# Performance work log

Hardware: AMD Instinct MI355X
Metric: run time of the kernel (lower is better)

Reference implementation:

```python
import jax, jax.numpy as jnp
import numpy as np


def setup_inputs() -> dict:
    key = jax.random.key(0)
    B, L, D, N = 2, 2048, 1024, 16
    ks = jax.random.split(key, 8)
    s = 1.0 / np.sqrt(D)
    # S4D-real init for A_log, matching the module
    A_log = jnp.log(jnp.broadcast_to(jnp.arange(1, N + 1, dtype=jnp.float32), (D, N)))
    return {
        "x": jax.random.normal(ks[0], (B, L, D), jnp.float32),
        "Wz": jax.random.normal(ks[1], (D, D), jnp.float32) * s,
        "bz": jnp.zeros((D,), jnp.float32),
        "Wx": jax.random.normal(ks[2], (D, D), jnp.float32) * s,
        "bx": jnp.zeros((D,), jnp.float32),
        "WB": jax.random.normal(ks[3], (D, N), jnp.float32) * s,
        "bB": jnp.zeros((N,), jnp.float32),
        "WC": jax.random.normal(ks[4], (D, N), jnp.float32) * s,
        "bC": jnp.zeros((N,), jnp.float32),
        "Wdt": jax.random.normal(ks[5], (D, D), jnp.float32) * s,
        "bdt": jnp.zeros((D,), jnp.float32),
        "A_log": A_log,
        "Wout": jax.random.normal(ks[6], (D, D), jnp.float32) * s,
        "bout": jnp.zeros((D,), jnp.float32),
    }


def reference(x, Wz, bz, Wx, bx, WB, bB, WC, bC, Wdt, bdt, A_log, Wout, bout):
    B, L, D = x.shape
    N = A_log.shape[1]

    # input-dependent projections
    z = jax.nn.sigmoid(x @ Wz + bz)            # (B,L,D) gate
    x_ssm = x @ Wx + bx                        # (B,L,D)
    Bm = x @ WB + bB                           # (B,L,N)
    C = x @ WC + bC                            # (B,L,N)
    dt = jax.nn.softplus(x @ Wdt + bdt)        # (B,L,D)

    A = -jnp.exp(A_log)                        # (D,N)
    A_bar = jnp.exp(dt[..., None] * A)         # (B,L,D,N) discretized state matrix
    # x_db = x_ssm * (dt * B)  -> (B,L,D,N)
    x_db = x_ssm[..., None] * (dt[..., None] * Bm[..., None, :])

    # scan over time: move L to leading axis
    a_scan = jnp.transpose(A_bar, (1, 0, 2, 3))   # (L,B,D,N)
    x_scan = jnp.transpose(x_db, (1, 0, 2, 3))    # (L,B,D,N)
    c_scan = jnp.transpose(C, (1, 0, 2))          # (L,B,N)

    def ssm_step(h, inp):
        a_t, x_t, c_t = inp                       # (B,D,N),(B,D,N),(B,N)
        h_new = a_t * h + x_t
        y_t = jnp.einsum('bdn,bn->bd', h_new, c_t)
        return h_new, y_t

    h0 = jnp.zeros((B, D, N), x.dtype)
    _, y_ssm = jax.lax.scan(ssm_step, h0, (a_scan, x_scan, c_scan))
    y_ssm = jnp.transpose(y_ssm, (1, 0, 2))       # (B,L,D)

    y = y_ssm * z
    return y @ Wout + bout
```

## Files before the change

kernel.cpp:

```cpp
#include <hip/hip_runtime.h>
#include <math.h>

#define CHUNKS 64
#define LCH    32

#define GBM 128
#define GBN 128
#define GBK 32
#define ATILE (GBM * GBK)
#define BTILE (GBN * GBK)

typedef __attribute__((ext_vector_type(8))) short bf16x8;
typedef __attribute__((ext_vector_type(4))) float f32x4;
typedef __attribute__((ext_vector_type(8))) unsigned short us8;
typedef __attribute__((ext_vector_type(4))) unsigned short us4;

typedef __attribute__((address_space(1))) const unsigned int gu32;
typedef __attribute__((address_space(3))) unsigned int lu32;

__device__ __forceinline__ void gload16(const unsigned short* g, unsigned short* l) {
    __builtin_amdgcn_global_load_lds((gu32*)g, (lu32*)l, 16, 0, 0);
}

__device__ __forceinline__ unsigned short f2bf(float f) {
    unsigned int u = __float_as_uint(f);
    unsigned int r = (u + 0x7FFFu + ((u >> 16) & 1u)) >> 16;
    return (unsigned short)r;
}

__global__ __launch_bounds__(256) void convert_bf16(
    const float* __restrict__ in, unsigned short* __restrict__ out, int n4)
{
    int i = blockIdx.x * 256 + threadIdx.x;
    if (i < n4) {
        float4 v = ((const float4*)in)[i];
        us4 u;
        u[0] = f2bf(v.x); u[1] = f2bf(v.y); u[2] = f2bf(v.z); u[3] = f2bf(v.w);
        ((us4*)out)[i] = u;
    }
}

__global__ __launch_bounds__(256) void transpose4_bf16(
    const float* __restrict__ W0, const float* __restrict__ W1,
    const float* __restrict__ W2, const float* __restrict__ W3,
    unsigned short* __restrict__ T0, unsigned short* __restrict__ T1,
    unsigned short* __restrict__ T2, unsigned short* __restrict__ T3, int D)
{
    const float* W = (blockIdx.z == 0) ? W0 : (blockIdx.z == 1) ? W1
                   : (blockIdx.z == 2) ? W2 : W3;
    unsigned short* Wt = (blockIdx.z == 0) ? T0 : (blockIdx.z == 1) ? T1
                       : (blockIdx.z == 2) ? T2 : T3;

    __shared__ float Ls[64][65];
    const int n0 = blockIdx.x * 64;
    const int k0 = blockIdx.y * 64;
    const int tx = threadIdx.x;

#pragma unroll
    for (int i = 0; i < 4; i++) {
        int idx = tx + i * 256;
        int kr = idx >> 4;
        int ng = idx & 15;
        float4 v = *(const float4*)&W[(size_t)(k0 + kr) * D + n0 + ng * 4];
        Ls[kr][ng * 4 + 0] = v.x;
        Ls[kr][ng * 4 + 1] = v.y;
        Ls[kr][ng * 4 + 2] = v.z;
        Ls[kr][ng * 4 + 3] = v.w;
    }
    __syncthreads();
#pragma unroll
    for (int i = 0; i < 4; i++) {
        int idx = tx + i * 256;
        int nr = idx >> 4;
        int kg = idx & 15;
        us4 u;
#pragma unroll
        for (int j = 0; j < 4; j++) u[j] = f2bf(Ls[kg * 4 + j][nr]);
        *(us4*)&Wt[(size_t)(n0 + nr) * D + k0 + kg * 4] = u;
    }
}

__device__ __forceinline__ void stage_tile(
    const unsigned short* __restrict__ A, const unsigned short* __restrict__ B,
    unsigned short* As, unsigned short* Bs,
    int brow, int bcol, int K, int k0, int wave, int srow, int sq)
{
    gload16(&A[(size_t)(brow + wave * 32      + srow) * K + k0 + sq],
            &As[(wave * 32) * GBK]);
    gload16(&A[(size_t)(brow + wave * 32 + 16 + srow) * K + k0 + sq],
            &As[(wave * 32 + 16) * GBK]);
    gload16(&B[(size_t)(bcol + wave * 32      + srow) * K + k0 + sq],
            &Bs[(wave * 32) * GBK]);
    gload16(&B[(size_t)(bcol + wave * 32 + 16 + srow) * K + k0 + sq],
            &Bs[(wave * 32 + 16) * GBK]);
}

__device__ __forceinline__ void gemm_core(
    const unsigned short* __restrict__ A, const unsigned short* __restrict__ B,
    unsigned short* As, unsigned short* Bs,
    int brow, int bcol, int K, f32x4 acc[4][4],
    int wave, int lane, int wr, int wc, int lrow, int lk)
{
    const int srow = lane >> 2;
    const int sq   = ((lane & 3) ^ ((lane >> 3) & 3)) * 8;

#pragma unroll
    for (int m = 0; m < 4; m++)
#pragma unroll
        for (int n = 0; n < 4; n++) acc[m][n] = (f32x4)(0.f);

    const int nk = K / GBK;
    stage_tile(A, B, As,         Bs,         brow, bcol, K, 0,   wave, srow, sq);
    stage_tile(A, B, As + ATILE, Bs + BTILE, brow, bcol, K, GBK, wave, srow, sq);

    int cur = 0;
    int nxt = 2;
    for (int kt = 0; kt < nk; ++kt) {
        if (kt + 2 < nk) {
            stage_tile(A, B, As + nxt * ATILE, Bs + nxt * BTILE,
                       brow, bcol, K, (kt + 2) * GBK, wave, srow, sq);
            asm volatile("s_waitcnt vmcnt(8)" ::: "memory");
        } else if (kt + 1 < nk) {
            asm volatile("s_waitcnt vmcnt(4)" ::: "memory");
        } else {
            asm volatile("s_waitcnt vmcnt(0)" ::: "memory");
        }
        __builtin_amdgcn_s_barrier();

        const unsigned short* as = As + cur * ATILE;
        const unsigned short* bs = Bs + cur * BTILE;

        bf16x8 av[4], bv[4];
#pragma unroll
        for (int m = 0; m < 4; m++) {
            int row = wr * 64 + m * 16 + lrow;
            av[m] = *(const bf16x8*)&as[row * GBK + ((lk ^ ((row >> 1) & 3)) * 8)];
        }
#pragma unroll
        for (int n = 0; n < 4; n++) {
            int row = wc * 64 + n * 16 + lrow;
            bv[n] = *(const bf16x8*)&bs[row * GBK + ((lk ^ ((row >> 1) & 3)) * 8)];
        }
#pragma unroll
        for (int m = 0; m < 4; m++)
#pragma unroll
            for (int n = 0; n < 4; n++)
                acc[m][n] = __builtin_amdgcn_mfma_f32_16x16x32_bf16(
                    av[m], bv[n], acc[m][n], 0, 0, 0);

        asm volatile("s_waitcnt lgkmcnt(0)" ::: "memory");
        __builtin_amdgcn_s_barrier();
        cur = (cur == 2) ? 0 : cur + 1;
        nxt = (nxt == 2) ? 0 : nxt + 1;
    }
}

__global__ __launch_bounds__(256) void proj3_gemm(
    const unsigned short* __restrict__ A,
    const unsigned short* __restrict__ W0, const unsigned short* __restrict__ W1,
    const unsigned short* __restrict__ W2,
    const float* __restrict__ b0, const float* __restrict__ b1,
    const float* __restrict__ b2,
    float* __restrict__ o0, float* __restrict__ o1, float* __restrict__ o2,
    int K, int Nc)
{
    __shared__ unsigned short As[3 * ATILE];
    __shared__ unsigned short Bs[3 * BTILE];

    const int bid = blockIdx.x;
    const int idx = bid >> 3;
    const int by  = (bid & 7) * 4 + idx / 24;
    const int bx  = idx % 24;

    const int widx = bx >> 3;
    const unsigned short* B = (widx == 0) ? W0 : (widx == 1) ? W1 : W2;
    const float* bias = (widx == 0) ? b0 : (widx == 1) ? b1 : b2;
    float* out = (widx == 0) ? o0 : (widx == 1) ? o1 : o2;

    const int tx = threadIdx.x;
    const int wave = tx >> 6;
    const int lane = tx & 63;
    const int wr = wave >> 1, wc = wave & 1;
    const int lrow = lane & 15, lk = lane >> 4;
    const int brow = by * GBM;
    const int bcol = (bx & 7) * GBN;

    f32x4 acc[4][4];
    gemm_core(A, B, As, Bs, brow, bcol, K, acc, wave, lane, wr, wc, lrow, lk);

#pragma unroll
    for (int n = 0; n < 4; n++) {
        int col = bcol + wc * 64 + n * 16 + lrow;
        float bval = bias[col];
#pragma unroll
        for (int m = 0; m < 4; m++) {
#pragma unroll
            for (int r = 0; r < 4; r++) {
                int row = brow + wr * 64 + m * 16 + lk * 4 + r;
                float v = acc[m][n][r] + bval;
                if (widx == 0) v = 1.f / (1.f + __expf(-v));
                else if (widx == 2) v = (v > 20.f) ? v : log1pf(__expf(v));
                out[(size_t)row * Nc + col] = v;
            }
        }
    }
}

__global__ __launch_bounds__(256) void gemm_bt(
    const unsigned short* __restrict__ A, const unsigned short* __restrict__ B,
    const float* __restrict__ bias, float* __restrict__ out, int K, int ldo)
{
    __shared__ unsigned short As[3 * ATILE];
    __shared__ unsigned short Bs[3 * BTILE];

    const int bid = blockIdx.x;
    const int idx = bid >> 3;
    const int by  = (bid & 7) * 4 + idx / 8;
    const int bx  = idx % 8;

    const int tx = threadIdx.x;
    const int wave = tx >> 6;
    const int lane = tx & 63;
    const int wr = wave >> 1, wc = wave & 1;
    const int lrow = lane & 15, lk = lane >> 4;
    const int brow = by * GBM;
    const int bcol = bx * GBN;

    f32x4 acc[4][4];
    gemm_core(A, B, As, Bs, brow, bcol, K, acc, wave, lane, wr, wc, lrow, lk);

#pragma unroll
    for (int n = 0; n < 4; n++) {
        int col = bcol + wc * 64 + n * 16 + lrow;
        float bval = bias[col];
#pragma unroll
        for (int m = 0; m < 4; m++) {
#pragma unroll
            for (int r = 0; r < 4; r++) {
                int row = brow + wr * 64 + m * 16 + lk * 4 + r;
                out[(size_t)row * ldo + col] = acc[m][n][r] + bval;
            }
        }
    }
}

__global__ __launch_bounds__(256) void bc_proj(
    const float* __restrict__ x,
    const float* __restrict__ WB, const float* __restrict__ bB,
    const float* __restrict__ WC, const float* __restrict__ bC,
    float* __restrict__ BC, int K, int M)
{
    __shared__ unsigned short Wl[32 * 1024];

    const int tx = threadIdx.x;

#pragma unroll
    for (int i = 0; i < 16; i++) {
        int e = tx + i * 256;
        int k = e >> 2;
        int n0 = (e & 3) * 4;
        float4 v = ((const float4*)WB)[e];
        float vv[4] = {v.x, v.y, v.z, v.w};
#pragma unroll
        for (int j = 0; j < 4; j++) {
            int n = n0 + j;
            Wl[n * 1024 + (((k & ~7) ^ ((n & 15) << 3)) | (k & 7))] = f2bf(vv[j]);
        }
    }
#pragma unroll
    for (int i = 0; i < 16; i++) {
        int e = tx + i * 256;
        int k = e >> 2;
        int n0 = (e & 3) * 4;
        float4 v = ((const float4*)WC)[e];
        float vv[4] = {v.x, v.y, v.z, v.w};
#pragma unroll
        for (int j = 0; j < 4; j++) {
            int n = 16 + n0 + j;
            Wl[n * 1024 + (((k & ~7) ^ ((n & 15) << 3)) | (k & 7))] = f2bf(vv[j]);
        }
    }
    __syncthreads();

    const int n = tx & 31;
    const int r = tx >> 5;
    const int row = blockIdx.x * 8 + r;

    const unsigned short* wrow = &Wl[n * 1024];
    const int sw = (n & 15) << 3;
    const float* xrow = &x[(size_t)row * K];

    float acc = 0.f;
    for (int kb = 0; kb < K; kb += 8) {
        us8 w8 = *(const us8*)&wrow[kb ^ sw];
        float4 xa = *(const float4*)&xrow[kb];
        float4 xb = *(const float4*)&xrow[kb + 4];
        float xv[8] = {xa.x, xa.y, xa.z, xa.w, xb.x, xb.y, xb.z, xb.w};
#pragma unroll
        for (int j = 0; j < 8; j++) {
            acc = fmaf(xv[j], __uint_as_float((unsigned)(unsigned short)w8[j] << 16), acc);
        }
    }

    float bias = (n < 16) ? bB[n] : bC[n - 16];
    BC[(size_t)row * 32 + n] = acc + bias;
}

__global__ __launch_bounds__(256) void scan_phase1(
    const float* __restrict__ xs, const float* __restrict__ dt,
    const float* __restrict__ BC, const float* __restrict__ A_log,
    float* __restrict__ P, float* __restrict__ Hl, int L, int D, int M)
{
    const int tx = threadIdx.x;
    const int d  = blockIdx.x * 256 + tx;
    const int c  = blockIdx.y;
    const int b  = blockIdx.z;
    const int m0 = b * L + c * LCH;

    __shared__ float bcs[LCH][32];
    {
        int row = tx >> 3, col = (tx & 7) * 4;
        *(f32x4*)&bcs[row][col] = *(const f32x4*)&BC[(size_t)(m0 + row) * 32 + col];
    }
    __syncthreads();

    float Av[16];
#pragma unroll
    for (int i = 0; i < 4; i++) {
        f32x4 a4 = *(const f32x4*)&A_log[d * 16 + i * 4];
#pragma unroll
        for (int j = 0; j < 4; j++) Av[i * 4 + j] = -__expf(a4[j]);
    }

    float h[16];
#pragma unroll
    for (int n = 0; n < 16; n++) h[n] = 0.f;
    float dts = 0.f;

    const size_t base = (size_t)m0 * D + d;
    float dtv = dt[base], xv = xs[base];
    for (int t = 0; t < LCH; t++) {
        float dtn = 0.f, xvn = 0.f;
        if (t + 1 < LCH) {
            dtn = dt[base + (size_t)(t + 1) * D];
            xvn = xs[base + (size_t)(t + 1) * D];
        }
        float xdt = xv * dtv;
        dts += dtv;
        f32x4 bm[4];
#pragma unroll
        for (int i = 0; i < 4; i++) bm[i] = *(const f32x4*)&bcs[t][i * 4];
#pragma unroll
        for (int n = 0; n < 16; n++) {
            float a = __expf(dtv * Av[n]);
            h[n] = fmaf(a, h[n], xdt * bm[n >> 2][n & 3]);
        }
        dtv = dtn; xv = xvn;
    }

    size_t idx = (((size_t)b * D + d) * CHUNKS + c) * 16;
#pragma unroll
    for (int i = 0; i < 4; i++) {
        f32x4 p4, h4;
#pragma unroll
        for (int j = 0; j < 4; j++) {
            p4[j] = __expf(Av[i * 4 + j] * dts);
            h4[j] = h[i * 4 + j];
        }
        *(f32x4*)&P[idx + i * 4]  = p4;
        *(f32x4*)&Hl[idx + i * 4] = h4;
    }
}

__global__ __launch_bounds__(256) void scan_phase2(
    const float* __restrict__ P, float* __restrict__ Hl, int D, int N)
{
    const int tid = blockIdx.x * 256 + threadIdx.x;
    const int n = tid & 15;
    const int dd = (tid >> 4) & 1023;
    const int b = tid >> 14;

    size_t base = (((size_t)b * D + dd) * CHUNKS) * 16 + n;
    float run = 0.f;
#pragma unroll 4
    for (int c = 0; c < CHUNKS; c++) {
        float p   = P[base + (size_t)c * 16];
        float tmp = Hl[base + (size_t)c * 16];
        Hl[base + (size_t)c * 16] = run;
        run = fmaf(p, run, tmp);
    }
}

__global__ __launch_bounds__(256) void scan_phase3(
    const float* __restrict__ xs, const float* __restrict__ dt,
    const float* __restrict__ BC, const float* __restrict__ z,
    const float* __restrict__ A_log, const float* __restrict__ Hin,
    unsigned short* __restrict__ ybf, int L, int D, int M)
{
    const int tx = threadIdx.x;
    const int d  = blockIdx.x * 256 + tx;
    const int c  = blockIdx.y;
    const int b  = blockIdx.z;
    const int m0 = b * L + c * LCH;

    __shared__ float bcs[LCH][32];
    {
        int row = tx >> 3, col = (tx & 7) * 4;
        *(f32x4*)&bcs[row][col] = *(const f32x4*)&BC[(size_t)(m0 + row) * 32 + col];
    }
    __syncthreads();

    float Av[16];
#pragma unroll
    for (int i = 0; i < 4; i++) {
        f32x4 a4 = *(const f32x4*)&A_log[d * 16 + i * 4];
#pragma unroll
        for (int j = 0; j < 4; j++) Av[i * 4 + j] = -__expf(a4[j]);
    }

    float h[16];
    {
        size_t hidx = (((size_t)b * D + d) * CHUNKS + c) * 16;
#pragma unroll
        for (int i = 0; i < 4; i++) {
            f32x4 h4 = *(const f32x4*)&Hin[hidx + i * 4];
#pragma unroll
            for (int j = 0; j < 4; j++) h[i * 4 + j] = h4[j];
        }
    }

    const size_t base = (size_t)m0 * D + d;
    float dtv = dt[base], xv = xs[base], zv = z[base];
    for (int t = 0; t < LCH; t++) {
        float dtn = 0.f, xvn = 0.f, zvn = 0.f;
        if (t + 1 < LCH) {
            dtn = dt[base + (size_t)(t + 1) * D];
            xvn = xs[base + (size_t)(t + 1) * D];
            zvn = z[base + (size_t)(t + 1) * D];
        }
        float xdt = xv * dtv;
        f32x4 bm[4], cm[4];
#pragma unroll
        for (int i = 0; i < 4; i++) {
            bm[i] = *(const f32x4*)&bcs[t][i * 4];
            cm[i] = *(const f32x4*)&bcs[t][16 + i * 4];
        }
        float y = 0.f;
#pragma unroll
        for (int n = 0; n < 16; n++) {
            float a = __expf(dtv * Av[n]);
            h[n] = fmaf(a, h[n], xdt * bm[n >> 2][n & 3]);
            y = fmaf(h[n], cm[n >> 2][n & 3], y);
        }
        ybf[base + (size_t)t * D] = f2bf(y * zv);
        dtv = dtn; xv = xvn; zv = zvn;
    }
}

extern "C" void kernel_launch(void* const* d_in, const int* in_sizes, int n_in,
                              void* d_out, int out_size, void* d_ws, size_t ws_size,
                              hipStream_t stream) {
    const float* x     = (const float*)d_in[0];
    const float* Wz    = (const float*)d_in[1];
    const float* bz    = (const float*)d_in[2];
    const float* Wx    = (const float*)d_in[3];
    const float* bx    = (const float*)d_in[4];
    const float* WB    = (const float*)d_in[5];
    const float* bB    = (const float*)d_in[6];
    const float* WC    = (const float*)d_in[7];
    const float* bC    = (const float*)d_in[8];
    const float* Wdt   = (const float*)d_in[9];
    const float* bdt   = (const float*)d_in[10];
    const float* A_log = (const float*)d_in[11];
    const float* Wout  = (const float*)d_in[12];
    const float* bout  = (const float*)d_in[13];
    float* out = (float*)d_out;

    const int Bb = 2, L = 2048, D = 1024, N = 16;
    const int M = Bb * L;
    const size_t MD = (size_t)M * D;

    float* ws   = (float*)d_ws;
    float* xsb  = ws;
    float* dtb  = xsb + MD;
    float* BCb  = dtb + MD;
    float* Pb   = BCb + (size_t)M * 32;
    float* Hlb  = Pb  + (size_t)Bb * D * CHUNKS * 16;
    unsigned short* xbf   = (unsigned short*)(Hlb + (size_t)Bb * D * CHUNKS * 16);
    unsigned short* Wzt   = xbf + MD;
    unsigned short* Wxt   = Wzt + (size_t)D * D;
    unsigned short* Wdtt  = Wxt + (size_t)D * D;
    unsigned short* Woutt = Wdtt + (size_t)D * D;
    float* zb = out;

    dim3 blk(256);
    dim3 gridT(D / 64, D / 64, 4);

    convert_bf16<<<dim3((unsigned)(MD / 4 / 256)), blk, 0, stream>>>(x, xbf, (int)(MD / 4));
    transpose4_bf16<<<gridT, blk, 0, stream>>>(Wz, Wx, Wdt, Wout,
                                               Wzt, Wxt, Wdtt, Woutt, D);

    proj3_gemm<<<dim3(3 * (D / GBN) * (M / GBM)), blk, 0, stream>>>(
        xbf, Wzt, Wxt, Wdtt, bz, bx, bdt, zb, xsb, dtb, D, D);
    bc_proj<<<dim3(M / 8), blk, 0, stream>>>(x, WB, bB, WC, bC, BCb, D, M);

    dim3 gridScan(D / 256, CHUNKS, Bb);
    scan_phase1<<<gridScan, blk, 0, stream>>>(xsb, dtb, BCb, A_log, Pb, Hlb, L, D, M);
    scan_phase2<<<dim3(Bb * D * N / 256), blk, 0, stream>>>(Pb, Hlb, D, N);
    scan_phase3<<<gridScan, blk, 0, stream>>>(xsb, dtb, BCb, zb, A_log, Hlb,
                                              xbf , L, D, M);

    gemm_bt<<<dim3((D / GBN) * (M / GBM)), blk, 0, stream>>>(xbf, Woutt, bout, out, D, D);
}
```

Measured before the change: 166.6 us.

## Store projection intermediates as bf16 and fuse x conversion into bc_proj

The z, x_ssm and dt intermediates written by the projection GEMM are now stored as bf16 instead of fp32, which halves the bytes written there and read back by the scan phases. The separate fp32-to-bf16 conversion kernel for x is removed, and bc_proj now does that conversion while it already reads x, so it must launch before the projection GEMM. This saves one launch and one pass over x, at the cost of lower precision on dt and x_ssm feeding the recurrence, which could push error closer to tolerance.

```diff
diff --git a/kernel.cpp b/kernel.cpp
--- a/kernel.cpp
+++ b/kernel.cpp
@@ -27,17 +27,8 @@
     unsigned int r = (u + 0x7FFFu + ((u >> 16) & 1u)) >> 16;
     return (unsigned short)r;
 }
-
-__global__ __launch_bounds__(256) void convert_bf16(
-    const float* __restrict__ in, unsigned short* __restrict__ out, int n4)
-{
-    int i = blockIdx.x * 256 + threadIdx.x;
-    if (i < n4) {
-        float4 v = ((const float4*)in)[i];
-        us4 u;
-        u[0] = f2bf(v.x); u[1] = f2bf(v.y); u[2] = f2bf(v.z); u[3] = f2bf(v.w);
-        ((us4*)out)[i] = u;
-    }
+__device__ __forceinline__ float bf2f(unsigned short u) {
+    return __uint_as_float((unsigned)u << 16);
 }
 
 __global__ __launch_bounds__(256) void transpose4_bf16(
@@ -161,7 +152,8 @@
     const unsigned short* __restrict__ W2,
     const float* __restrict__ b0, const float* __restrict__ b1,
     const float* __restrict__ b2,
-    float* __restrict__ o0, float* __restrict__ o1, float* __restrict__ o2,
+    unsigned short* __restrict__ o0, unsigned short* __restrict__ o1,
+    unsigned short* __restrict__ o2,
     int K, int Nc)
 {
     __shared__ unsigned short As[3 * ATILE];
@@ -175,7 +167,7 @@
     const int widx = bx >> 3;
     const unsigned short* B = (widx == 0) ? W0 : (widx == 1) ? W1 : W2;
     const float* bias = (widx == 0) ? b0 : (widx == 1) ? b1 : b2;
-    float* out = (widx == 0) ? o0 : (widx == 1) ? o1 : o2;
+    unsigned short* out = (widx == 0) ? o0 : (widx == 1) ? o1 : o2;
 
     const int tx = threadIdx.x;
     const int wave = tx >> 6;
@@ -200,7 +192,7 @@
                 float v = acc[m][n][r] + bval;
                 if (widx == 0) v = 1.f / (1.f + __expf(-v));
                 else if (widx == 2) v = (v > 20.f) ? v : log1pf(__expf(v));
-                out[(size_t)row * Nc + col] = v;
+                out[(size_t)row * Nc + col] = f2bf(v);
             }
         }
     }
@@ -248,7 +240,7 @@
     const float* __restrict__ x,
     const float* __restrict__ WB, const float* __restrict__ bB,
     const float* __restrict__ WC, const float* __restrict__ bC,
-    float* __restrict__ BC, int K, int M)
+    float* __restrict__ BC, unsigned short* __restrict__ xbf, int K, int M)
 {
     __shared__ unsigned short Wl[32 * 1024];
 
@@ -280,6 +272,20 @@
             Wl[n * 1024 + (((k & ~7) ^ ((n & 15) << 3)) | (k & 7))] = f2bf(vv[j]);
         }
     }
+
+#pragma unroll
+    for (int i = 0; i < 4; i++) {
+        int e = tx + i * 256;
+        int rr = e >> 7;
+        int cc = (e & 127) * 8;
+        const float* src = &x[(size_t)(blockIdx.x * 8 + rr) * K + cc];
+        float4 a = *(const float4*)src;
+        float4 b = *(const float4*)(src + 4);
+        us8 u;
+        u[0] = f2bf(a.x); u[1] = f2bf(a.y); u[2] = f2bf(a.z); u[3] = f2bf(a.w);
+        u[4] = f2bf(b.x); u[5] = f2bf(b.y); u[6] = f2bf(b.z); u[7] = f2bf(b.w);
+        *(us8*)&xbf[(size_t)(blockIdx.x * 8 + rr) * K + cc] = u;
+    }
     __syncthreads();
 
     const int n = tx & 31;
@@ -307,7 +313,7 @@
 }
 
 __global__ __launch_bounds__(256) void scan_phase1(
-    const float* __restrict__ xs, const float* __restrict__ dt,
+    const unsigned short* __restrict__ xs, const unsigned short* __restrict__ dt,
     const float* __restrict__ BC, const float* __restrict__ A_log,
     float* __restrict__ P, float* __restrict__ Hl, int L, int D, int M)
 {
@@ -338,12 +344,12 @@
     float dts = 0.f;
 
     const size_t base = (size_t)m0 * D + d;
-    float dtv = dt[base], xv = xs[base];
+    float dtv = bf2f(dt[base]), xv = bf2f(xs[base]);
     for (int t = 0; t < LCH; t++) {
         float dtn = 0.f, xvn = 0.f;
         if (t + 1 < LCH) {
-            dtn = dt[base + (size_t)(t + 1) * D];
-            xvn = xs[base + (size_t)(t + 1) * D];
+            dtn = bf2f(dt[base + (size_t)(t + 1) * D]);
+            xvn = bf2f(xs[base + (size_t)(t + 1) * D]);
         }
         float xdt = xv * dtv;
         dts += dtv;
@@ -392,8 +398,8 @@
 }
 
 __global__ __launch_bounds__(256) void scan_phase3(
-    const float* __restrict__ xs, const float* __restrict__ dt,
-    const float* __restrict__ BC, const float* __restrict__ z,
+    const unsigned short* __restrict__ xs, const unsigned short* __restrict__ dt,
+    const float* __restrict__ BC, const unsigned short* __restrict__ z,
     const float* __restrict__ A_log, const float* __restrict__ Hin,
     unsigned short* __restrict__ ybf, int L, int D, int M)
 {
@@ -430,13 +436,13 @@
     }
 
     const size_t base = (size_t)m0 * D + d;
-    float dtv = dt[base], xv = xs[base], zv = z[base];
+    float dtv = bf2f(dt[base]), xv = bf2f(xs[base]), zv = bf2f(z[base]);
     for (int t = 0; t < LCH; t++) {
         float dtn = 0.f, xvn = 0.f, zvn = 0.f;
         if (t + 1 < LCH) {
-            dtn = dt[base + (size_t)(t + 1) * D];
-            xvn = xs[base + (size_t)(t + 1) * D];
-            zvn = z[base + (size_t)(t + 1) * D];
+            dtn = bf2f(dt[base + (size_t)(t + 1) * D]);
+            xvn = bf2f(xs[base + (size_t)(t + 1) * D]);
+            zvn = bf2f(z[base + (size_t)(t + 1) * D]);
         }
         float xdt = xv * dtv;
         f32x4 bm[4], cm[4];
@@ -480,10 +486,10 @@
     const int M = Bb * L;
     const size_t MD = (size_t)M * D;
 
-    float* ws   = (float*)d_ws;
-    float* xsb  = ws;
-    float* dtb  = xsb + MD;
-    float* BCb  = dtb + MD;
+    unsigned short* ws16 = (unsigned short*)d_ws;
+    unsigned short* xsb  = ws16;
+    unsigned short* dtb  = xsb + MD;
+    float* BCb  = (float*)(dtb + MD);
     float* Pb   = BCb + (size_t)M * 32;
     float* Hlb  = Pb  + (size_t)Bb * D * CHUNKS * 16;
     unsigned short* xbf   = (unsigned short*)(Hlb + (size_t)Bb * D * CHUNKS * 16);
@@ -491,18 +497,17 @@
     unsigned short* Wxt   = Wzt + (size_t)D * D;
     unsigned short* Wdtt  = Wxt + (size_t)D * D;
     unsigned short* Woutt = Wdtt + (size_t)D * D;
-    float* zb = out;
+    unsigned short* zb = (unsigned short*)out;
 
     dim3 blk(256);
     dim3 gridT(D / 64, D / 64, 4);
 
-    convert_bf16<<<dim3((unsigned)(MD / 4 / 256)), blk, 0, stream>>>(x, xbf, (int)(MD / 4));
     transpose4_bf16<<<gridT, blk, 0, stream>>>(Wz, Wx, Wdt, Wout,
                                                Wzt, Wxt, Wdtt, Woutt, D);
+    bc_proj<<<dim3(M / 8), blk, 0, stream>>>(x, WB, bB, WC, bC, BCb, xbf, D, M);
 
     proj3_gemm<<<dim3(3 * (D / GBN) * (M / GBM)), blk, 0, stream>>>(
         xbf, Wzt, Wxt, Wdtt, bz, bx, bdt, zb, xsb, dtb, D, D);
-    bc_proj<<<dim3(M / 8), blk, 0, stream>>>(x, WB, bB, WC, bC, BCb, D, M);
 
     dim3 gridScan(D / 256, CHUNKS, Bb);
     scan_phase1<<<gridScan, blk, 0, stream>>>(xsb, dtb, BCb, A_log, Pb, Hlb, L, D, M);
```

New measurement: 154.3 us (median of 2 runs). 1.08x faster.
